# Optimization experiments

Measured on AMD Instinct MI355X. Metric: run time of the kernel, lower is better.

The kernel has to match this reference:

```python
import jax, jax.numpy as jnp
import numpy as np

B, A, T = 256, 512, 21
DIM = 128
SC = 6
NHEAD, HD = 4, DIM // 4

def conv1d_relu(x, w, b, stride=2):
    # x: (N, C, L), w: (O, I, K)
    y = jax.lax.conv_general_dilated(x, w, (stride,), 'SAME', dimension_numbers=('NCH', 'OIH', 'NCH'))
    return jax.nn.relu(y + b[None, :, None])

def to_vector(feat, vm):
    vec_mask = vm[..., :-1] & vm[..., 1:]
    while vec_mask.ndim < feat.ndim:
        vec_mask = vec_mask[..., None]
    return jnp.where(vec_mask, feat[:, :, 1:] - feat[:, :, :-1], jnp.zeros_like(feat[:, :, 1:]))

def setup_inputs():
    key = jax.random.key(0)
    ks = jax.random.split(key, 24)
    f32 = jnp.float32
    inp = {}
    inp['position'] = jax.random.normal(ks[0], (B, A, T, 2), f32)
    inp['heading'] = jax.random.normal(ks[1], (B, A, T), f32)
    inp['velocity'] = jax.random.normal(ks[2], (B, A, T, 2), f32)
    inp['shape'] = jax.random.uniform(ks[3], (B, A, T, 2), f32)
    inp['current_state'] = jax.random.normal(ks[4], (B, SC), f32)
    inp['category'] = jax.random.randint(ks[5], (B, A), 0, 4)
    inp['valid_mask'] = jax.random.randint(ks[6], (B, A, T), 0, 2).astype(bool)
    # history encoder (CNN) params: 9 -> 32 -> 64 -> 128 channels, k=3, stride 2
    inp['conv1_w'] = jax.random.normal(ks[7], (32, 9, 3), f32) * 0.1
    inp['conv1_b'] = jnp.zeros((32,), f32)
    inp['conv2_w'] = jax.random.normal(ks[8], (64, 32, 3), f32) * 0.1
    inp['conv2_b'] = jnp.zeros((64,), f32)
    inp['conv3_w'] = jax.random.normal(ks[9], (128, 64, 3), f32) * 0.1
    inp['conv3_b'] = jnp.zeros((128,), f32)
    # StateAttentionEncoder params
    inp['se_w'] = jax.random.normal(ks[10], (SC, DIM), f32) * 0.02   # per-channel Linear(1,dim) weights
    inp['se_b'] = jnp.zeros((SC, DIM), f32)
    inp['pos_embed'] = jax.random.normal(ks[11], (1, SC, DIM), f32) * 0.02
    inp['query'] = jax.random.normal(ks[12], (1, 1, DIM), f32) * 0.02
    inp['in_proj_w'] = jax.random.normal(ks[13], (3 * DIM, DIM), f32) * (1.0 / np.sqrt(DIM))
    inp['in_proj_b'] = jnp.zeros((3 * DIM,), f32)
    inp['out_proj_w'] = jax.random.normal(ks[14], (DIM, DIM), f32) * (1.0 / np.sqrt(DIM))
    inp['out_proj_b'] = jnp.zeros((DIM,), f32)
    inp['type_emb'] = jax.random.normal(ks[15], (4, DIM), f32) * 0.02
    return inp

def reference(position, heading, velocity, shape, current_state, category, valid_mask,
              conv1_w, conv1_b, conv2_w, conv2_b, conv3_w, conv3_b,
              se_w, se_b, pos_embed, query, in_proj_w, in_proj_b, out_proj_w, out_proj_b,
              type_emb):
    # --- build per-step agent features (B, A, T-1, 9) ---
    heading_vec = to_vector(heading, valid_mask)
    valid_mask_vec = valid_mask[..., 1:] & valid_mask[..., :-1]
    agent_feature = jnp.concatenate([
        to_vector(position, valid_mask),
        to_vector(velocity, valid_mask),
        jnp.stack([jnp.cos(heading_vec), jnp.sin(heading_vec)], axis=-1),
        shape[:, :, 1:],
        valid_mask_vec.astype(jnp.float32)[..., None],
    ], axis=-1)
    bs, nA, Tm1, C = agent_feature.shape
    x = agent_feature.reshape(bs * nA, Tm1, C).transpose(0, 2, 1)  # (N, 9, T-1)
    # --- history CNN encoder (applied to all rows, then masked; same math as boolean gather/scatter) ---
    h = conv1d_relu(x, conv1_w, conv1_b)
    h = conv1d_relu(h, conv2_w, conv2_b)
    h = conv1d_relu(h, conv3_w, conv3_b)
    enc = h.mean(axis=-1)  # (N, DIM)
    valid_agent = valid_mask.any(-1).reshape(-1)
    x_agent = jnp.where(valid_agent[:, None], enc, 0.0).reshape(bs, nA, DIM)
    # --- ego state attention encoder (eval mode: no token dropout) ---
    ego = current_state[:, :SC]
    x_embed = ego[:, :, None] * se_w[None] + se_b[None] + pos_embed  # (B, SC, DIM)
    Wq, Wk, Wv = in_proj_w[:DIM], in_proj_w[DIM:2 * DIM], in_proj_w[2 * DIM:]
    bq, bk, bv = in_proj_b[:DIM], in_proj_b[DIM:2 * DIM], in_proj_b[2 * DIM:]
    q = (query[0, 0] @ Wq.T + bq).reshape(NHEAD, HD)             # (H, D)
    k = (x_embed @ Wk.T + bk).reshape(bs, SC, NHEAD, HD)          # (B, S, H, D)
    v = (x_embed @ Wv.T + bv).reshape(bs, SC, NHEAD, HD)
    scores = jnp.einsum('hd,bshd->bhs', q, k) * (1.0 / np.sqrt(HD))
    attn = jax.nn.softmax(scores, axis=-1)
    o = jnp.einsum('bhs,bshd->bhd', attn, v).reshape(bs, DIM)
    x_ego = o @ out_proj_w.T + out_proj_b                         # (B, DIM)
    x_agent = x_agent.at[:, 0].set(x_ego)
    # --- type embedding add ---
    return x_agent + type_emb[category]
```

## Files before the change

### kernel.cpp

```cpp
#include <hip/hip_runtime.h>
#include <hip/hip_bf16.h>


#define BB 256
#define AAG 512
#define TT 21
#define NAG (BB * AAG)

typedef __hip_bfloat16 bf16;
typedef __attribute__((ext_vector_type(8))) short s8v;
typedef __attribute__((ext_vector_type(4))) float f4v;

__device__ int g_dtype;
__device__ int g_mask_mode;
__device__ __align__(16) short g_w1p[32 * 64];
__device__ __align__(16) short g_w2p[64 * 96];
__device__ __align__(16) short g_w3p[128 * 192];
__device__ __align__(16) float g_b1[32];
__device__ __align__(16) float g_b2[64];
__device__ __align__(16) float g_b3[128];
__device__ __align__(16) float g_wqk[4 * 128];
__device__ __align__(16) float g_qb[4];

template <int DT>
__device__ __forceinline__ float ldf(const void* p, long i) {
    if (DT) return __bfloat162float(((const bf16*)p)[i]);
    return ((const float*)p)[i];
}
template <int DT>
__device__ __forceinline__ void stf(void* p, long i, float v) {
    if (DT) ((bf16*)p)[i] = __float2bfloat16(v);
    else    ((float*)p)[i] = v;
}
__device__ __forceinline__ unsigned short f2bu(float x) {
    bf16 b = __float2bfloat16(x);
    union { bf16 b; unsigned short u; } cv; cv.b = b; return cv.u;
}
__device__ __forceinline__ float bu2f(unsigned short u) {
    union { unsigned int i; float f; } cv; cv.i = ((unsigned int)u) << 16; return cv.f;
}
template <int DT>
__device__ __forceinline__ float2 ldf2(const void* p, long i) {
    if (DT) {
        unsigned int u = *(const unsigned int*)((const bf16*)p + i);
        return make_float2(bu2f((unsigned short)(u & 0xffffu)),
                           bu2f((unsigned short)(u >> 16)));
    }
    return *(const float2*)((const float*)p + i);
}
__device__ __forceinline__ bool mask_at(const void* p, long i, int mode) {
    if (mode == 0) return ((const int*)p)[i] != 0;
    if (mode == 1) return ((const unsigned char*)p)[i] != 0;
    if (mode == 2) return ((const float*)p)[i] != 0.f;
    return (((const unsigned short*)p)[i] & 0x7fff) != 0;
}

template <int DT>
__device__ __forceinline__ float rowdot64(const void* W, long off, const float* y) {
    float acc = 0.f;
    if (DT) {
        const unsigned short* wr = (const unsigned short*)W + off;
#pragma unroll
        for (int i = 0; i < 8; i++) {
            uint4 w = *(const uint4*)(wr + i * 8);
            acc = fmaf(bu2f((unsigned short)(w.x & 0xffffu)), y[i * 8 + 0], acc);
            acc = fmaf(bu2f((unsigned short)(w.x >> 16)),     y[i * 8 + 1], acc);
            acc = fmaf(bu2f((unsigned short)(w.y & 0xffffu)), y[i * 8 + 2], acc);
            acc = fmaf(bu2f((unsigned short)(w.y >> 16)),     y[i * 8 + 3], acc);
            acc = fmaf(bu2f((unsigned short)(w.z & 0xffffu)), y[i * 8 + 4], acc);
            acc = fmaf(bu2f((unsigned short)(w.z >> 16)),     y[i * 8 + 5], acc);
            acc = fmaf(bu2f((unsigned short)(w.w & 0xffffu)), y[i * 8 + 6], acc);
            acc = fmaf(bu2f((unsigned short)(w.w >> 16)),     y[i * 8 + 7], acc);
        }
    } else {
        const float* wr = (const float*)W + off;
#pragma unroll
        for (int i = 0; i < 16; i++) {
            float4 w = *(const float4*)(wr + i * 4);
            acc = fmaf(w.x, y[i * 4 + 0], acc);
            acc = fmaf(w.y, y[i * 4 + 1], acc);
            acc = fmaf(w.z, y[i * 4 + 2], acc);
            acc = fmaf(w.w, y[i * 4 + 3], acc);
        }
    }
    return acc;
}

template <int DT>
__device__ __forceinline__ void prep_body(const void* w1, const void* b1,
                                          const void* w2, const void* b2,
                                          const void* w3, const void* b3) {
    int tid = blockIdx.x * 256 + threadIdx.x;
    const int nt = 64 * 256;
    for (int i = tid; i < 32 * 64; i += nt) {
        int oc = i >> 6, k = i & 63, tap = k >> 4, ic = k & 15;
        float v = (tap < 3 && ic < 9) ? ldf<DT>(w1, oc * 27 + ic * 3 + tap) : 0.f;
        g_w1p[i] = (short)f2bu(v);
    }
    for (int i = tid; i < 64 * 96; i += nt) {
        int oc = i / 96, k = i % 96, tap = k >> 5, ic = k & 31;
        g_w2p[i] = (short)f2bu(ldf<DT>(w2, oc * 96 + ic * 3 + tap));
    }
    for (int i = tid; i < 128 * 192; i += nt) {
        int oc = i / 192, k = i % 192, tap = k >> 6, ic = k & 63;
        g_w3p[i] = (short)f2bu(ldf<DT>(w3, oc * 192 + ic * 3 + tap));
    }
    for (int i = tid; i < 32; i += nt) g_b1[i] = ldf<DT>(b1, i);
    for (int i = tid; i < 64; i += nt) g_b2[i] = ldf<DT>(b2, i);
    for (int i = tid; i < 128; i += nt) g_b3[i] = ldf<DT>(b3, i);
}

template <int DT>
__device__ __forceinline__ void qprep_body(const void* query, const void* ipw,
                                           const void* ipb, float* sq) {
    int tid = threadIdx.x;
    if (tid < 128) {
        float acc = ldf<DT>(ipb, tid);
        for (int e = 0; e < 128; e++)
            acc = fmaf(ldf<DT>(query, e), ldf<DT>(ipw, (long)tid * 128 + e), acc);
        sq[tid] = acc;
    }
    __syncthreads();
    int e = tid & 127, hb = tid >> 7;
    for (int h = hb; h < 4; h += 2) {
        float acc = 0.f;
#pragma unroll
        for (int j = 0; j < 32; j++)
            acc = fmaf(sq[h * 32 + j], ldf<DT>(ipw, (long)(128 + h * 32 + j) * 128 + e), acc);
        g_wqk[h * 128 + e] = acc;
    }
    if (tid < 4) {
        float acc = 0.f;
#pragma unroll
        for (int j = 0; j < 32; j++)
            acc = fmaf(sq[tid * 32 + j], ldf<DT>(ipb, 128 + tid * 32 + j), acc);
        g_qb[tid] = acc;
    }
}

__global__ __launch_bounds__(256) void prep_kernel(
    const unsigned int* __restrict__ pw, const unsigned char* __restrict__ m,
    const void* __restrict__ w1, const void* __restrict__ b1,
    const void* __restrict__ w2, const void* __restrict__ b2,
    const void* __restrict__ w3, const void* __restrict__ b3,
    const void* __restrict__ query, const void* __restrict__ ipw,
    const void* __restrict__ ipb) {
    __shared__ int cls[4];
    __shared__ int mv;
    __shared__ int good;
    __shared__ float sq[128];
    int tid = threadIdx.x;
    if (tid < 4) cls[tid] = 0;
    if (tid == 0) { mv = 0; good = 0; }
    __syncthreads();
    int g = 0;
    for (int i = tid; i < 1024; i += 256) {
        unsigned int w = pw[i];
        unsigned int h0 = w & 0xffffu, h1 = w >> 16;
        unsigned int e0 = (h0 >> 7) & 0xff, e1 = (h1 >> 7) & 0xff;
        if (h0 == 0 || (e0 >= 90 && e0 <= 160)) g++;
        if (h1 == 0 || (e1 >= 90 && e1 <= 160)) g++;
    }
    atomicAdd(&good, g);
    int l0 = 0, l1 = 0, l2 = 0, l3 = 0, lm = 0;
    for (int i = tid; i < 4096; i += 256) {
        int v = m[i];
        if (v) {
            switch (i & 3) { case 0: l0 = 1; break; case 1: l1 = 1; break;
                             case 2: l2 = 1; break; default: l3 = 1; }
            if (v > lm) lm = v;
        }
    }
    if (l0) atomicOr(&cls[0], 1);
    if (l1) atomicOr(&cls[1], 1);
    if (l2) atomicOr(&cls[2], 1);
    if (l3) atomicOr(&cls[3], 1);
    atomicMax(&mv, lm);
    __syncthreads();
    int dt = (good >= 1740) ? 1 : 0;
    int mode;
    if (!cls[1] && !cls[2] && !cls[3]) mode = 0;
    else if (!cls[0] && !cls[1])       mode = 2;
    else if (mv <= 1)                  mode = 1;
    else                               mode = 3;
    if (blockIdx.x == 0 && tid == 0) { g_dtype = dt; g_mask_mode = mode; }

    if (blockIdx.x < 64) {
        if (dt) prep_body<1>(w1, b1, w2, b2, w3, b3);
        else    prep_body<0>(w1, b1, w2, b2, w3, b3);
    } else {
        if (dt) qprep_body<1>(query, ipw, ipb, sq);
        else    qprep_body<0>(query, ipw, ipb, sq);
    }
}

#define FEAT_RS 24
#define FEAT_AS 568
#define H1_RS 40
#define H1_AS 440
#define H2_RS 72
#define H2_AS 504
#define C3_AS 392
#define OFF_H1 9088
#define OFF_VALID 32256
#define SMEM_BYTES 32320

#define MFMA16(a, b, c) __builtin_amdgcn_mfma_f32_16x16x32_bf16((a), (b), (c), 0, 0, 0)

template <int DT>
__device__ __forceinline__ void stage1_body(
    const void* pos, const void* heading, const void* vel, const void* shp,
    const void* vmask, const int* category, const void* type_emb, void* out,
    char* smem, long agent0) {
    short* feat = (short*)smem;
    short* h1   = (short*)smem + OFF_H1;
    short* h2   = (short*)smem;
    short* c3   = (short*)smem + OFF_H1;
    int* s_valid = (int*)(smem + OFF_VALID);

    const int tid = threadIdx.x;
    const int wave = tid >> 6, lane = tid & 63;
    const int col = lane & 15, quad = lane >> 4;
    const int mode = g_mask_mode;

    if (tid < 16) s_valid[tid] = 0;
    {
        unsigned int* h1u = (unsigned int*)h1;
        h1u[(tid >> 4) * 220 + 200 + (tid & 15)] = 0;
    }
    __syncthreads();

    for (int idx = tid; idx < 16 * 22; idx += 256) {
        int ag = idx / 22, t = idx % 22;
        short* row = feat + ag * FEAT_AS + t * FEAT_RS;
        if (t >= 20) {
            *(uint4*)row = make_uint4(0, 0, 0, 0);
            *(uint4*)(row + 8) = make_uint4(0, 0, 0, 0);
            if (t == 20) {
                long base = (agent0 + ag) * TT + 20;
                if (mask_at(vmask, base, mode)) atomicOr(&s_valid[ag], 1);
            }
        } else {
            long base = (agent0 + ag) * TT + t;
            bool vmt = mask_at(vmask, base, mode);
            if (vmt) atomicOr(&s_valid[ag], 1);
            bool m2 = vmt && mask_at(vmask, base + 1, mode);
            float2 pa = ldf2<DT>(pos, base * 2), pb = ldf2<DT>(pos, base * 2 + 2);
            float2 va = ldf2<DT>(vel, base * 2), vb = ldf2<DT>(vel, base * 2 + 2);
            float hh0 = ldf<DT>(heading, base), hh1 = ldf<DT>(heading, base + 1);
            float2 sv = ldf2<DT>(shp, base * 2 + 2);
            float dh = m2 ? (hh1 - hh0) : 0.f;
            float sn, cn;
            __sincosf(dh, &sn, &cn);
            unsigned int p0 = f2bu(m2 ? pb.x - pa.x : 0.f) | ((unsigned int)f2bu(m2 ? pb.y - pa.y : 0.f) << 16);
            unsigned int p1 = f2bu(m2 ? vb.x - va.x : 0.f) | ((unsigned int)f2bu(m2 ? vb.y - va.y : 0.f) << 16);
            unsigned int p2 = f2bu(cn) | ((unsigned int)f2bu(sn) << 16);
            unsigned int p3 = f2bu(sv.x) | ((unsigned int)f2bu(sv.y) << 16);
            unsigned int p4 = (unsigned int)f2bu(m2 ? 1.f : 0.f);
            *(uint4*)row = make_uint4(p0, p1, p2, p3);
            *(uint4*)(row + 8) = make_uint4(p4, 0, 0, 0);
        }
    }
    __syncthreads();

    {
        int Mt = wave >> 1;
        int oc = Mt * 16 + col;
        s8v a0 = *(const s8v*)(g_w1p + oc * 64 + quad * 8);
        s8v a1 = *(const s8v*)(g_w1p + oc * 64 + 32 + quad * 8);
        int k0 = quad * 8, k1 = 32 + quad * 8;
        int tap0 = k0 >> 4, ic0 = k0 & 15;
        int tap1 = k1 >> 4, ic1 = k1 & 15;
        int ocr = Mt * 16 + quad * 4;
        f4v bia = *(const f4v*)(g_b1 + ocr);
        int ag = col;
        const short* agbase = feat + ag * FEAT_AS;
#pragma unroll
        for (int i = 0; i < 5; i++) {
            int p = (wave & 1) * 5 + i;
            const short* bb = agbase + 2 * p * FEAT_RS;
            s8v b0 = *(const s8v*)(bb + tap0 * FEAT_RS + ic0);
            s8v b1 = *(const s8v*)(bb + tap1 * FEAT_RS + ic1);
            f4v acc = {0.f, 0.f, 0.f, 0.f};
            acc = MFMA16(a0, b0, acc);
            acc = MFMA16(a1, b1, acc);
            unsigned int lo = f2bu(fmaxf(acc[0] + bia[0], 0.f)) | ((unsigned int)f2bu(fmaxf(acc[1] + bia[1], 0.f)) << 16);
            unsigned int hi = f2bu(fmaxf(acc[2] + bia[2], 0.f)) | ((unsigned int)f2bu(fmaxf(acc[3] + bia[3], 0.f)) << 16);
            *(uint2*)(h1 + ag * H1_AS + p * H1_RS + ocr) = make_uint2(lo, hi);
        }
    }
    __syncthreads();

    {
        unsigned int* h2u = (unsigned int*)h2;
        for (int i = tid; i < 1024; i += 256) {
            int a2 = i >> 6, r = (i >> 5) & 1, cc = i & 31;
            h2u[a2 * 252 + r * 216 + cc] = 0;
        }
        int Mt = wave;
        int oc = Mt * 16 + col;
        s8v a[3];
#pragma unroll
        for (int ks = 0; ks < 3; ks++)
            a[ks] = *(const s8v*)(g_w2p + oc * 96 + ks * 32 + quad * 8);
        int ocr = Mt * 16 + quad * 4;
        f4v bia = *(const f4v*)(g_b2 + ocr);
        int ag = col;
#pragma unroll
        for (int p = 0; p < 5; p++) {
            f4v acc = {0.f, 0.f, 0.f, 0.f};
#pragma unroll
            for (int ks = 0; ks < 3; ks++) {
                s8v b = *(const s8v*)(h1 + ag * H1_AS + (2 * p + ks) * H1_RS + quad * 8);
                acc = MFMA16(a[ks], b, acc);
            }
            unsigned int lo = f2bu(fmaxf(acc[0] + bia[0], 0.f)) | ((unsigned int)f2bu(fmaxf(acc[1] + bia[1], 0.f)) << 16);
            unsigned int hi = f2bu(fmaxf(acc[2] + bia[2], 0.f)) | ((unsigned int)f2bu(fmaxf(acc[3] + bia[3], 0.f)) << 16);
            *(uint2*)(h2 + ag * H2_AS + (p + 1) * H2_RS + ocr) = make_uint2(lo, hi);
        }
    }
    __syncthreads();

#pragma unroll
    for (int m2 = 0; m2 < 2; m2++) {
        int Mt = wave * 2 + m2;
        int oc = Mt * 16 + col;
        s8v a[6];
#pragma unroll
        for (int ks = 0; ks < 6; ks++)
            a[ks] = *(const s8v*)(g_w3p + oc * 192 + ks * 32 + quad * 8);
        int ocr = Mt * 16 + quad * 4;
        f4v bia = *(const f4v*)(g_b3 + ocr);
        int ag = col;
#pragma unroll
        for (int p = 0; p < 3; p++) {
            f4v acc = {0.f, 0.f, 0.f, 0.f};
#pragma unroll
            for (int ks = 0; ks < 6; ks++) {
                int kg = ks * 32 + quad * 8;
                int tap = kg >> 6, ic = kg & 63;
                s8v b = *(const s8v*)(h2 + ag * H2_AS + (2 * p + tap) * H2_RS + ic);
                acc = MFMA16(a[ks], b, acc);
            }
            unsigned int lo = f2bu(fmaxf(acc[0] + bia[0], 0.f)) | ((unsigned int)f2bu(fmaxf(acc[1] + bia[1], 0.f)) << 16);
            unsigned int hi = f2bu(fmaxf(acc[2] + bia[2], 0.f)) | ((unsigned int)f2bu(fmaxf(acc[3] + bia[3], 0.f)) << 16);
            *(uint2*)(c3 + ag * C3_AS + p * 128 + ocr) = make_uint2(lo, hi);
        }
    }
    __syncthreads();

    {
        int ag = tid >> 4;
        int ocg = (tid & 15) * 8;
        const short* cb = c3 + ag * C3_AS;
        s8v x0 = *(const s8v*)(cb + ocg);
        s8v x1 = *(const s8v*)(cb + 128 + ocg);
        s8v x2 = *(const s8v*)(cb + 256 + ocg);
        int valid = s_valid[ag];
        long agl = agent0 + ag;
        bool skip = ((agl & (AAG - 1)) == 0);
        int cat = category[agl];
        float vals[8];
#pragma unroll
        for (int j = 0; j < 8; j++) {
            float m = (bu2f((unsigned short)x0[j]) + bu2f((unsigned short)x1[j]) +
                       bu2f((unsigned short)x2[j])) * (1.f / 3.f);
            vals[j] = valid ? m : 0.f;
        }
        if (!skip) {
            if (DT) {
                s8v te = *(const s8v*)((const bf16*)type_emb + (long)cat * 128 + ocg);
                s8v o;
#pragma unroll
                for (int j = 0; j < 8; j++)
                    o[j] = (short)f2bu(vals[j] + bu2f((unsigned short)te[j]));
                *(s8v*)((bf16*)out + agl * 128 + ocg) = o;
            } else {
                const float4* tep = (const float4*)((const float*)type_emb + (long)cat * 128 + ocg);
                float4 t0 = tep[0], t1 = tep[1];
                float4 o0 = make_float4(vals[0] + t0.x, vals[1] + t0.y, vals[2] + t0.z, vals[3] + t0.w);
                float4 o1 = make_float4(vals[4] + t1.x, vals[5] + t1.y, vals[6] + t1.z, vals[7] + t1.w);
                float4* op = (float4*)((float*)out + agl * 128 + ocg);
                op[0] = o0; op[1] = o1;
            }
        }
    }
}

template <int DT>
__device__ __forceinline__ void stage2_body(
    const void* cs, const int* category,
    const void* se_w, const void* se_b, const void* pe,
    const void* ipw, const void* ipb, const void* opw, const void* opb,
    const void* type_emb, void* out, char* smem) {
    const int b = blockIdx.x;
    const int tid = threadIdx.x;
    const int d = tid & 127, half = tid >> 7;

    float* s_xe  = (float*)smem;
    float* s_y   = s_xe + 768;
    float* s_sc  = s_y + 512;
    float* s_att = s_sc + 32;
    float* s_o   = s_att + 32;
    float* s_par = s_o + 128;

    for (int idx = tid; idx < 768; idx += 256) {
        int s = idx >> 7, dd = idx & 127;
        float ego = ldf<DT>(cs, b * 6 + s);
        s_xe[idx] = fmaf(ego, ldf<DT>(se_w, s * 128 + dd),
                         ldf<DT>(se_b, s * 128 + dd) + ldf<DT>(pe, s * 128 + dd));
    }
    __syncthreads();

    if (tid < 96) {
        int g = tid >> 2, lig = tid & 3;
        int h = g / 6, s = g - h * 6;
        const float* xr = s_xe + s * 128 + lig * 32;
        const float* wr = g_wqk + h * 128 + lig * 32;
        float t = 0.f;
#pragma unroll
        for (int e = 0; e < 32; e++) t = fmaf(xr[e], wr[e], t);
        t += __shfl_xor(t, 1, 4);
        t += __shfl_xor(t, 2, 4);
        if (lig == 0) s_sc[g] = (t + g_qb[h]) * 0.17677669529663687f;
    }
    __syncthreads();

    if (tid < 4) {
        float mx = -1e30f;
#pragma unroll
        for (int s = 0; s < 6; s++) mx = fmaxf(mx, s_sc[tid * 6 + s]);
        float sum = 0.f, ex[6];
#pragma unroll
        for (int s = 0; s < 6; s++) { ex[s] = expf(s_sc[tid * 6 + s] - mx); sum += ex[s]; }
        float inv = 1.f / sum;
#pragma unroll
        for (int s = 0; s < 6; s++) s_att[tid * 6 + s] = ex[s] * inv;
    }
    __syncthreads();

    for (int idx = tid; idx < 512; idx += 256) {
        int h = idx >> 7, e = idx & 127;
        float y = 0.f;
#pragma unroll
        for (int s = 0; s < 6; s++) y = fmaf(s_att[h * 6 + s], s_xe[s * 128 + e], y);
        s_y[idx] = y;
    }
    __syncthreads();

    {
        int h = d >> 5;
        const float* yr = s_y + h * 128 + half * 64;
        s_par[half * 128 + d] = rowdot64<DT>(ipw, (long)(256 + d) * 128 + half * 64, yr);
    }
    __syncthreads();
    if (half == 0) s_o[d] = s_par[d] + s_par[128 + d] + ldf<DT>(ipb, 256 + d);
    __syncthreads();

    {
        const float* orr = s_o + half * 64;
        s_par[half * 128 + d] = rowdot64<DT>(opw, (long)d * 128 + half * 64, orr);
    }
    __syncthreads();
    if (half == 0) {
        float x = s_par[d] + s_par[128 + d] + ldf<DT>(opb, d);
        int cat = category[(long)b * AAG];
        stf<DT>(out, (long)b * AAG * 128 + d, x + ldf<DT>(type_emb, cat * 128 + d));
    }
}

__global__ __launch_bounds__(256) void fused_kernel(
    const void* __restrict__ pos, const void* __restrict__ heading,
    const void* __restrict__ vel, const void* __restrict__ shp,
    const void* __restrict__ vmask, const int* __restrict__ category,
    const void* __restrict__ type_emb, void* __restrict__ out,
    const void* __restrict__ cs, const void* __restrict__ se_w,
    const void* __restrict__ se_b, const void* __restrict__ pe,
    const void* __restrict__ ipw, const void* __restrict__ ipb,
    const void* __restrict__ opw, const void* __restrict__ opb) {
    __shared__ __align__(16) char smem[SMEM_BYTES];
    if (blockIdx.x < BB) {
        if (g_dtype) stage2_body<1>(cs, category, se_w, se_b, pe, ipw, ipb, opw, opb, type_emb, out, smem);
        else         stage2_body<0>(cs, category, se_w, se_b, pe, ipw, ipb, opw, opb, type_emb, out, smem);
    } else {
        long agent0 = (long)(blockIdx.x - BB) * 16;
        if (g_dtype) stage1_body<1>(pos, heading, vel, shp, vmask, category, type_emb, out, smem, agent0);
        else         stage1_body<0>(pos, heading, vel, shp, vmask, category, type_emb, out, smem, agent0);
    }
}

extern "C" void kernel_launch(void* const* d_in, const int* in_sizes, int n_in,
                              void* d_out, int out_size, void* d_ws, size_t ws_size,
                              hipStream_t stream) {
    const void* position      = d_in[0];
    const void* heading       = d_in[1];
    const void* velocity      = d_in[2];
    const void* shape         = d_in[3];
    const void* current_state = d_in[4];
    const int*  category      = (const int*)d_in[5];
    const void* valid_mask    = d_in[6];
    const void* conv1_w = d_in[7];
    const void* conv1_b = d_in[8];
    const void* conv2_w = d_in[9];
    const void* conv2_b = d_in[10];
    const void* conv3_w = d_in[11];
    const void* conv3_b = d_in[12];
    const void* se_w    = d_in[13];
    const void* se_b    = d_in[14];
    const void* pos_embed = d_in[15];
    const void* query     = d_in[16];
    const void* in_proj_w = d_in[17];
    const void* in_proj_b = d_in[18];
    const void* out_proj_w = d_in[19];
    const void* out_proj_b = d_in[20];
    const void* type_emb   = d_in[21];

    hipLaunchKernelGGL(prep_kernel, dim3(65), dim3(256), 0, stream,
                       (const unsigned int*)position, (const unsigned char*)valid_mask,
                       conv1_w, conv1_b, conv2_w, conv2_b, conv3_w, conv3_b,
                       query, in_proj_w, in_proj_b);

    hipLaunchKernelGGL(fused_kernel, dim3(BB + NAG / 16), dim3(256), 0, stream,
                       position, heading, velocity, shape, valid_mask, category,
                       type_emb, d_out,
                       current_state, se_w, se_b, pos_embed,
                       in_proj_w, in_proj_b, out_proj_w, out_proj_b);
}
```

Before: 300.7 us.

## Fuse conv3 epilogue with temporal mean and output write, drop atomics

```diff
diff --git a/kernel.cpp b/kernel.cpp
--- a/kernel.cpp
+++ b/kernel.cpp
@@ -200,7 +200,6 @@
 #define H1_AS 440
 #define H2_RS 72
 #define H2_AS 504
-#define C3_AS 392
 #define OFF_H1 9088
 #define OFF_VALID 32256
 #define SMEM_BYTES 32320
@@ -215,7 +214,6 @@
     short* feat = (short*)smem;
     short* h1   = (short*)smem + OFF_H1;
     short* h2   = (short*)smem;
-    short* c3   = (short*)smem + OFF_H1;
     int* s_valid = (int*)(smem + OFF_VALID);
 
     const int tid = threadIdx.x;
@@ -223,27 +221,27 @@
     const int col = lane & 15, quad = lane >> 4;
     const int mode = g_mask_mode;
 
-    if (tid < 16) s_valid[tid] = 0;
     {
         unsigned int* h1u = (unsigned int*)h1;
         h1u[(tid >> 4) * 220 + 200 + (tid & 15)] = 0;
     }
-    __syncthreads();
-
     for (int idx = tid; idx < 16 * 22; idx += 256) {
         int ag = idx / 22, t = idx % 22;
         short* row = feat + ag * FEAT_AS + t * FEAT_RS;
+        if (t == 0) {
+            long b0 = (agent0 + ag) * TT;
+            int v = 0;
+#pragma unroll
+            for (int tt = 0; tt < TT; tt++)
+                v |= mask_at(vmask, b0 + tt, mode) ? 1 : 0;
+            s_valid[ag] = v;
+        }
         if (t >= 20) {
             *(uint4*)row = make_uint4(0, 0, 0, 0);
             *(uint4*)(row + 8) = make_uint4(0, 0, 0, 0);
-            if (t == 20) {
-                long base = (agent0 + ag) * TT + 20;
-                if (mask_at(vmask, base, mode)) atomicOr(&s_valid[ag], 1);
-            }
         } else {
             long base = (agent0 + ag) * TT + t;
             bool vmt = mask_at(vmask, base, mode);
-            if (vmt) atomicOr(&s_valid[ag], 1);
             bool m2 = vmt && mask_at(vmask, base + 1, mode);
             float2 pa = ldf2<DT>(pos, base * 2), pb = ldf2<DT>(pos, base * 2 + 2);
             float2 va = ldf2<DT>(vel, base * 2), vb = ldf2<DT>(vel, base * 2 + 2);
@@ -321,67 +319,56 @@
     }
     __syncthreads();
 
-#pragma unroll
-    for (int m2 = 0; m2 < 2; m2++) {
-        int Mt = wave * 2 + m2;
-        int oc = Mt * 16 + col;
-        s8v a[6];
-#pragma unroll
-        for (int ks = 0; ks < 6; ks++)
-            a[ks] = *(const s8v*)(g_w3p + oc * 192 + ks * 32 + quad * 8);
-        int ocr = Mt * 16 + quad * 4;
-        f4v bia = *(const f4v*)(g_b3 + ocr);
+    {
         int ag = col;
-#pragma unroll
-        for (int p = 0; p < 3; p++) {
-            f4v acc = {0.f, 0.f, 0.f, 0.f};
-#pragma unroll
-            for (int ks = 0; ks < 6; ks++) {
-                int kg = ks * 32 + quad * 8;
-                int tap = kg >> 6, ic = kg & 63;
-                s8v b = *(const s8v*)(h2 + ag * H2_AS + (2 * p + tap) * H2_RS + ic);
-                acc = MFMA16(a[ks], b, acc);
-            }
-            unsigned int lo = f2bu(fmaxf(acc[0] + bia[0], 0.f)) | ((unsigned int)f2bu(fmaxf(acc[1] + bia[1], 0.f)) << 16);
-            unsigned int hi = f2bu(fmaxf(acc[2] + bia[2], 0.f)) | ((unsigned int)f2bu(fmaxf(acc[3] + bia[3], 0.f)) << 16);
-            *(uint2*)(c3 + ag * C3_AS + p * 128 + ocr) = make_uint2(lo, hi);
-        }
-    }
-    __syncthreads();
-
-    {
-        int ag = tid >> 4;
-        int ocg = (tid & 15) * 8;
-        const short* cb = c3 + ag * C3_AS;
-        s8v x0 = *(const s8v*)(cb + ocg);
-        s8v x1 = *(const s8v*)(cb + 128 + ocg);
-        s8v x2 = *(const s8v*)(cb + 256 + ocg);
-        int valid = s_valid[ag];
         long agl = agent0 + ag;
         bool skip = ((agl & (AAG - 1)) == 0);
+        int valid = s_valid[ag];
         int cat = category[agl];
-        float vals[8];
-#pragma unroll
-        for (int j = 0; j < 8; j++) {
-            float m = (bu2f((unsigned short)x0[j]) + bu2f((unsigned short)x1[j]) +
-                       bu2f((unsigned short)x2[j])) * (1.f / 3.f);
-            vals[j] = valid ? m : 0.f;
-        }
-        if (!skip) {
-            if (DT) {
-                s8v te = *(const s8v*)((const bf16*)type_emb + (long)cat * 128 + ocg);
-                s8v o;
-#pragma unroll
-                for (int j = 0; j < 8; j++)
-                    o[j] = (short)f2bu(vals[j] + bu2f((unsigned short)te[j]));
-                *(s8v*)((bf16*)out + agl * 128 + ocg) = o;
-            } else {
-                const float4* tep = (const float4*)((const float*)type_emb + (long)cat * 128 + ocg);
-                float4 t0 = tep[0], t1 = tep[1];
-                float4 o0 = make_float4(vals[0] + t0.x, vals[1] + t0.y, vals[2] + t0.z, vals[3] + t0.w);
-                float4 o1 = make_float4(vals[4] + t1.x, vals[5] + t1.y, vals[6] + t1.z, vals[7] + t1.w);
-                float4* op = (float4*)((float*)out + agl * 128 + ocg);
-                op[0] = o0; op[1] = o1;
+#pragma unroll
+        for (int m2 = 0; m2 < 2; m2++) {
+            int Mt = wave * 2 + m2;
+            int oc = Mt * 16 + col;
+            s8v a[6];
+#pragma unroll
+            for (int ks = 0; ks < 6; ks++)
+                a[ks] = *(const s8v*)(g_w3p + oc * 192 + ks * 32 + quad * 8);
+            int ocr = Mt * 16 + quad * 4;
+            f4v bia = *(const f4v*)(g_b3 + ocr);
+            f4v macc = {0.f, 0.f, 0.f, 0.f};
+#pragma unroll
+            for (int p = 0; p < 3; p++) {
+                f4v acc = {0.f, 0.f, 0.f, 0.f};
+#pragma unroll
+                for (int ks = 0; ks < 6; ks++) {
+                    int kg = ks * 32 + quad * 8;
+                    int tap = kg >> 6, ic = kg & 63;
+                    s8v b = *(const s8v*)(h2 + ag * H2_AS + (2 * p + tap) * H2_RS + ic);
+                    acc = MFMA16(a[ks], b, acc);
+                }
+#pragma unroll
+                for (int j = 0; j < 4; j++)
+                    macc[j] += fmaxf(acc[j] + bia[j], 0.f);
+            }
+            if (!skip) {
+                float vals[4];
+#pragma unroll
+                for (int j = 0; j < 4; j++)
+                    vals[j] = valid ? macc[j] * (1.f / 3.f) : 0.f;
+                if (DT) {
+                    const unsigned short* tep = (const unsigned short*)type_emb + (long)cat * 128 + ocr;
+                    uint2 te = *(const uint2*)tep;
+                    unsigned int lo = f2bu(vals[0] + bu2f((unsigned short)(te.x & 0xffffu))) |
+                                      ((unsigned int)f2bu(vals[1] + bu2f((unsigned short)(te.x >> 16))) << 16);
+                    unsigned int hi = f2bu(vals[2] + bu2f((unsigned short)(te.y & 0xffffu))) |
+                                      ((unsigned int)f2bu(vals[3] + bu2f((unsigned short)(te.y >> 16))) << 16);
+                    *(uint2*)((bf16*)out + agl * 128 + ocr) = make_uint2(lo, hi);
+                } else {
+                    float4 te = *(const float4*)((const float*)type_emb + (long)cat * 128 + ocr);
+                    float4 o = make_float4(vals[0] + te.x, vals[1] + te.y,
+                                           vals[2] + te.z, vals[3] + te.w);
+                    *(float4*)((float*)out + agl * 128 + ocr) = o;
+                }
             }
         }
     }
@@ -469,7 +456,7 @@
     }
 }
 
-__global__ __launch_bounds__(256) void fused_kernel(
+__global__ __launch_bounds__(256, 8) void fused_kernel(
     const void* __restrict__ pos, const void* __restrict__ heading,
     const void* __restrict__ vel, const void* __restrict__ shp,
     const void* __restrict__ vmask, const int* __restrict__ category,
```

After: 369.6 us. 22.9% more time.

## Shrink stage-1 agent batch to 12 and split ego attention into separate kernel

Applied to the files above, without the earlier changes.

```diff
diff --git a/kernel.cpp b/kernel.cpp
--- a/kernel.cpp
+++ b/kernel.cpp
@@ -6,6 +6,8 @@
 #define AAG 512
 #define TT 21
 #define NAG (BB * AAG)
+#define AB 12
+#define NB1 ((NAG + AB - 1) / AB)
 
 typedef __hip_bfloat16 bf16;
 typedef __attribute__((ext_vector_type(8))) short s8v;
@@ -201,9 +203,9 @@
 #define H2_RS 72
 #define H2_AS 504
 #define C3_AS 392
-#define OFF_H1 9088
-#define OFF_VALID 32256
-#define SMEM_BYTES 32320
+#define OFF_H1 6816
+#define OFF_VALID 24192
+#define SMEM_BYTES 24240
 
 #define MFMA16(a, b, c) __builtin_amdgcn_mfma_f32_16x16x32_bf16((a), (b), (c), 0, 0, 0)
 
@@ -221,29 +223,34 @@
     const int tid = threadIdx.x;
     const int wave = tid >> 6, lane = tid & 63;
     const int col = lane & 15, quad = lane >> 4;
+    const int cg = col < AB ? col : AB - 1;
     const int mode = g_mask_mode;
 
-    if (tid < 16) s_valid[tid] = 0;
-    {
+    if (tid < AB * 16) {
         unsigned int* h1u = (unsigned int*)h1;
         h1u[(tid >> 4) * 220 + 200 + (tid & 15)] = 0;
     }
-    __syncthreads();
-
-    for (int idx = tid; idx < 16 * 22; idx += 256) {
+    for (int idx = tid; idx < AB * 22; idx += 256) {
         int ag = idx / 22, t = idx % 22;
+        long agl = agent0 + ag;
+        bool live = agl < NAG;
         short* row = feat + ag * FEAT_AS + t * FEAT_RS;
-        if (t >= 20) {
+        if (t == 0) {
+            int v = 0;
+            if (live) {
+                long b0 = agl * TT;
+#pragma unroll
+                for (int tt = 0; tt < TT; tt++)
+                    v |= mask_at(vmask, b0 + tt, mode) ? 1 : 0;
+            }
+            s_valid[ag] = v;
+        }
+        if (t >= 20 || !live) {
             *(uint4*)row = make_uint4(0, 0, 0, 0);
             *(uint4*)(row + 8) = make_uint4(0, 0, 0, 0);
-            if (t == 20) {
-                long base = (agent0 + ag) * TT + 20;
-                if (mask_at(vmask, base, mode)) atomicOr(&s_valid[ag], 1);
-            }
         } else {
-            long base = (agent0 + ag) * TT + t;
+            long base = agl * TT + t;
             bool vmt = mask_at(vmask, base, mode);
-            if (vmt) atomicOr(&s_valid[ag], 1);
             bool m2 = vmt && mask_at(vmask, base + 1, mode);
             float2 pa = ldf2<DT>(pos, base * 2), pb = ldf2<DT>(pos, base * 2 + 2);
             float2 va = ldf2<DT>(vel, base * 2), vb = ldf2<DT>(vel, base * 2 + 2);
@@ -273,8 +280,7 @@
         int tap1 = k1 >> 4, ic1 = k1 & 15;
         int ocr = Mt * 16 + quad * 4;
         f4v bia = *(const f4v*)(g_b1 + ocr);
-        int ag = col;
-        const short* agbase = feat + ag * FEAT_AS;
+        const short* agbase = feat + cg * FEAT_AS;
 #pragma unroll
         for (int i = 0; i < 5; i++) {
             int p = (wave & 1) * 5 + i;
@@ -284,16 +290,18 @@
             f4v acc = {0.f, 0.f, 0.f, 0.f};
             acc = MFMA16(a0, b0, acc);
             acc = MFMA16(a1, b1, acc);
-            unsigned int lo = f2bu(fmaxf(acc[0] + bia[0], 0.f)) | ((unsigned int)f2bu(fmaxf(acc[1] + bia[1], 0.f)) << 16);
-            unsigned int hi = f2bu(fmaxf(acc[2] + bia[2], 0.f)) | ((unsigned int)f2bu(fmaxf(acc[3] + bia[3], 0.f)) << 16);
-            *(uint2*)(h1 + ag * H1_AS + p * H1_RS + ocr) = make_uint2(lo, hi);
+            if (col < AB) {
+                unsigned int lo = f2bu(fmaxf(acc[0] + bia[0], 0.f)) | ((unsigned int)f2bu(fmaxf(acc[1] + bia[1], 0.f)) << 16);
+                unsigned int hi = f2bu(fmaxf(acc[2] + bia[2], 0.f)) | ((unsigned int)f2bu(fmaxf(acc[3] + bia[3], 0.f)) << 16);
+                *(uint2*)(h1 + col * H1_AS + p * H1_RS + ocr) = make_uint2(lo, hi);
+            }
         }
     }
     __syncthreads();
 
     {
         unsigned int* h2u = (unsigned int*)h2;
-        for (int i = tid; i < 1024; i += 256) {
+        for (int i = tid; i < AB * 64; i += 256) {
             int a2 = i >> 6, r = (i >> 5) & 1, cc = i & 31;
             h2u[a2 * 252 + r * 216 + cc] = 0;
         }
@@ -305,18 +313,19 @@
             a[ks] = *(const s8v*)(g_w2p + oc * 96 + ks * 32 + quad * 8);
         int ocr = Mt * 16 + quad * 4;
         f4v bia = *(const f4v*)(g_b2 + ocr);
-        int ag = col;
 #pragma unroll
         for (int p = 0; p < 5; p++) {
             f4v acc = {0.f, 0.f, 0.f, 0.f};
 #pragma unroll
             for (int ks = 0; ks < 3; ks++) {
-                s8v b = *(const s8v*)(h1 + ag * H1_AS + (2 * p + ks) * H1_RS + quad * 8);
+                s8v b = *(const s8v*)(h1 + cg * H1_AS + (2 * p + ks) * H1_RS + quad * 8);
                 acc = MFMA16(a[ks], b, acc);
             }
-            unsigned int lo = f2bu(fmaxf(acc[0] + bia[0], 0.f)) | ((unsigned int)f2bu(fmaxf(acc[1] + bia[1], 0.f)) << 16);
-            unsigned int hi = f2bu(fmaxf(acc[2] + bia[2], 0.f)) | ((unsigned int)f2bu(fmaxf(acc[3] + bia[3], 0.f)) << 16);
-            *(uint2*)(h2 + ag * H2_AS + (p + 1) * H2_RS + ocr) = make_uint2(lo, hi);
+            if (col < AB) {
+                unsigned int lo = f2bu(fmaxf(acc[0] + bia[0], 0.f)) | ((unsigned int)f2bu(fmaxf(acc[1] + bia[1], 0.f)) << 16);
+                unsigned int hi = f2bu(fmaxf(acc[2] + bia[2], 0.f)) | ((unsigned int)f2bu(fmaxf(acc[3] + bia[3], 0.f)) << 16);
+                *(uint2*)(h2 + col * H2_AS + (p + 1) * H2_RS + ocr) = make_uint2(lo, hi);
+            }
         }
     }
     __syncthreads();
@@ -331,7 +340,6 @@
             a[ks] = *(const s8v*)(g_w3p + oc * 192 + ks * 32 + quad * 8);
         int ocr = Mt * 16 + quad * 4;
         f4v bia = *(const f4v*)(g_b3 + ocr);
-        int ag = col;
 #pragma unroll
         for (int p = 0; p < 3; p++) {
             f4v acc = {0.f, 0.f, 0.f, 0.f};
@@ -339,35 +347,36 @@
             for (int ks = 0; ks < 6; ks++) {
                 int kg = ks * 32 + quad * 8;
                 int tap = kg >> 6, ic = kg & 63;
-                s8v b = *(const s8v*)(h2 + ag * H2_AS + (2 * p + tap) * H2_RS + ic);
+                s8v b = *(const s8v*)(h2 + cg * H2_AS + (2 * p + tap) * H2_RS + ic);
                 acc = MFMA16(a[ks], b, acc);
             }
-            unsigned int lo = f2bu(fmaxf(acc[0] + bia[0], 0.f)) | ((unsigned int)f2bu(fmaxf(acc[1] + bia[1], 0.f)) << 16);
-            unsigned int hi = f2bu(fmaxf(acc[2] + bia[2], 0.f)) | ((unsigned int)f2bu(fmaxf(acc[3] + bia[3], 0.f)) << 16);
-            *(uint2*)(c3 + ag * C3_AS + p * 128 + ocr) = make_uint2(lo, hi);
-        }
-    }
-    __syncthreads();
-
-    {
+            if (col < AB) {
+                unsigned int lo = f2bu(fmaxf(acc[0] + bia[0], 0.f)) | ((unsigned int)f2bu(fmaxf(acc[1] + bia[1], 0.f)) << 16);
+                unsigned int hi = f2bu(fmaxf(acc[2] + bia[2], 0.f)) | ((unsigned int)f2bu(fmaxf(acc[3] + bia[3], 0.f)) << 16);
+                *(uint2*)(c3 + col * C3_AS + p * 128 + ocr) = make_uint2(lo, hi);
+            }
+        }
+    }
+    __syncthreads();
+
+    if (tid < AB * 16) {
         int ag = tid >> 4;
         int ocg = (tid & 15) * 8;
-        const short* cb = c3 + ag * C3_AS;
-        s8v x0 = *(const s8v*)(cb + ocg);
-        s8v x1 = *(const s8v*)(cb + 128 + ocg);
-        s8v x2 = *(const s8v*)(cb + 256 + ocg);
-        int valid = s_valid[ag];
         long agl = agent0 + ag;
-        bool skip = ((agl & (AAG - 1)) == 0);
-        int cat = category[agl];
-        float vals[8];
-#pragma unroll
-        for (int j = 0; j < 8; j++) {
-            float m = (bu2f((unsigned short)x0[j]) + bu2f((unsigned short)x1[j]) +
-                       bu2f((unsigned short)x2[j])) * (1.f / 3.f);
-            vals[j] = valid ? m : 0.f;
-        }
-        if (!skip) {
+        if (agl < NAG) {
+            const short* cb = c3 + ag * C3_AS;
+            s8v x0 = *(const s8v*)(cb + ocg);
+            s8v x1 = *(const s8v*)(cb + 128 + ocg);
+            s8v x2 = *(const s8v*)(cb + 256 + ocg);
+            int valid = s_valid[ag];
+            int cat = category[agl];
+            float vals[8];
+#pragma unroll
+            for (int j = 0; j < 8; j++) {
+                float m = (bu2f((unsigned short)x0[j]) + bu2f((unsigned short)x1[j]) +
+                           bu2f((unsigned short)x2[j])) * (1.f / 3.f);
+                vals[j] = valid ? m : 0.f;
+            }
             if (DT) {
                 s8v te = *(const s8v*)((const bf16*)type_emb + (long)cat * 128 + ocg);
                 s8v o;
@@ -387,17 +396,28 @@
     }
 }
 
+__global__ __launch_bounds__(256) void stage1_kernel(
+    const void* __restrict__ pos, const void* __restrict__ heading,
+    const void* __restrict__ vel, const void* __restrict__ shp,
+    const void* __restrict__ vmask, const int* __restrict__ category,
+    const void* __restrict__ type_emb, void* __restrict__ out) {
+    __shared__ __align__(16) char smem[SMEM_BYTES];
+    long agent0 = (long)blockIdx.x * AB;
+    if (g_dtype) stage1_body<1>(pos, heading, vel, shp, vmask, category, type_emb, out, smem, agent0);
+    else         stage1_body<0>(pos, heading, vel, shp, vmask, category, type_emb, out, smem, agent0);
+}
+
 template <int DT>
 __device__ __forceinline__ void stage2_body(
     const void* cs, const int* category,
     const void* se_w, const void* se_b, const void* pe,
     const void* ipw, const void* ipb, const void* opw, const void* opb,
-    const void* type_emb, void* out, char* smem) {
+    const void* type_emb, void* out, float* sm) {
     const int b = blockIdx.x;
     const int tid = threadIdx.x;
     const int d = tid & 127, half = tid >> 7;
 
-    float* s_xe  = (float*)smem;
+    float* s_xe  = sm;
     float* s_y   = s_xe + 768;
     float* s_sc  = s_y + 512;
     float* s_att = s_sc + 32;
@@ -469,24 +489,16 @@
     }
 }
 
-__global__ __launch_bounds__(256) void fused_kernel(
-    const void* __restrict__ pos, const void* __restrict__ heading,
-    const void* __restrict__ vel, const void* __restrict__ shp,
-    const void* __restrict__ vmask, const int* __restrict__ category,
-    const void* __restrict__ type_emb, void* __restrict__ out,
-    const void* __restrict__ cs, const void* __restrict__ se_w,
-    const void* __restrict__ se_b, const void* __restrict__ pe,
+__global__ __launch_bounds__(256) void stage2_kernel(
+    const void* __restrict__ cs, const int* __restrict__ category,
+    const void* __restrict__ se_w, const void* __restrict__ se_b,
+    const void* __restrict__ pe,
     const void* __restrict__ ipw, const void* __restrict__ ipb,
-    const void* __restrict__ opw, const void* __restrict__ opb) {
-    __shared__ __align__(16) char smem[SMEM_BYTES];
-    if (blockIdx.x < BB) {
-        if (g_dtype) stage2_body<1>(cs, category, se_w, se_b, pe, ipw, ipb, opw, opb, type_emb, out, smem);
-        else         stage2_body<0>(cs, category, se_w, se_b, pe, ipw, ipb, opw, opb, type_emb, out, smem);
-    } else {
-        long agent0 = (long)(blockIdx.x - BB) * 16;
-        if (g_dtype) stage1_body<1>(pos, heading, vel, shp, vmask, category, type_emb, out, smem, agent0);
-        else         stage1_body<0>(pos, heading, vel, shp, vmask, category, type_emb, out, smem, agent0);
-    }
+    const void* __restrict__ opw, const void* __restrict__ opb,
+    const void* __restrict__ type_emb, void* __restrict__ out) {
+    __shared__ float sm[1728];
+    if (g_dtype) stage2_body<1>(cs, category, se_w, se_b, pe, ipw, ipb, opw, opb, type_emb, out, sm);
+    else         stage2_body<0>(cs, category, se_w, se_b, pe, ipw, ipb, opw, opb, type_emb, out, sm);
 }
 
 extern "C" void kernel_launch(void* const* d_in, const int* in_sizes, int n_in,
@@ -520,9 +532,11 @@
                        conv1_w, conv1_b, conv2_w, conv2_b, conv3_w, conv3_b,
                        query, in_proj_w, in_proj_b);
 
-    hipLaunchKernelGGL(fused_kernel, dim3(BB + NAG / 16), dim3(256), 0, stream,
+    hipLaunchKernelGGL(stage1_kernel, dim3(NB1), dim3(256), 0, stream,
                        position, heading, velocity, shape, valid_mask, category,
-                       type_emb, d_out,
-                       current_state, se_w, se_b, pos_embed,
-                       in_proj_w, in_proj_b, out_proj_w, out_proj_b);
-}
+                       type_emb, d_out);
+
+    hipLaunchKernelGGL(stage2_kernel, dim3(BB), dim3(256), 0, stream,
+                       current_state, category, se_w, se_b, pos_embed,
+                       in_proj_w, in_proj_b, out_proj_w, out_proj_b, type_emb, d_out);
+}
```

Result: slower. 331.9 us (+10.4%).
